# Kernel tuning notes

Measured on AMD Instinct MI355X. Metric: run time of the kernel, lower is better.

Reference implementation:

```python
import jax, jax.numpy as jnp
import numpy as np

N = 50000
E = 1600000
IN_DIM = 256
HID = 64
OUT = 16
NEG_SLOPE = 0.01


def setup_inputs() -> dict:
    key = jax.random.key(0)
    ks = jax.random.split(key, 6)
    local_features = jax.random.normal(ks[0], (N, IN_DIM), dtype=jnp.float32)
    edge_index = jax.random.randint(ks[1], (2, E), 0, N, dtype=jnp.int32)
    W0 = jax.random.normal(ks[2], (IN_DIM, HID), dtype=jnp.float32) * 0.05
    a0 = jax.random.normal(ks[3], (2 * HID, 1), dtype=jnp.float32) * 0.05
    W1 = jax.random.normal(ks[4], (HID, OUT), dtype=jnp.float32) * 0.05
    a1 = jax.random.normal(ks[5], (2 * OUT, 1), dtype=jnp.float32) * 0.05
    return {"local_features": local_features, "edge_index": edge_index,
            "W0": W0, "a0": a0, "W1": W1, "a1": a1}


def _segment_softmax(scores, seg, num_segments):
    # softmax over edges sharing the same row (destination) id
    smax = jax.ops.segment_max(scores, seg, num_segments=num_segments)
    ex = jnp.exp(scores - smax[seg])
    ssum = jax.ops.segment_sum(ex, seg, num_segments=num_segments)
    return ex / ssum[seg]


def _gat_layer(H, row, col, W, a, apply_elu):
    d = W.shape[1]
    Hw = H @ W                                   # [N, d]
    # score_e = leaky_relu([Hw[row] || Hw[col]] @ a) = leaky_relu(pr[row] + pc[col])
    pr = Hw @ a[:d, 0]                           # [N]
    pc = Hw @ a[d:, 0]                           # [N]
    s = pr[row] + pc[col]                        # [E]
    s = jnp.where(s >= 0, s, NEG_SLOPE * s)      # leaky_relu
    att = _segment_softmax(s, row, Hw.shape[0])  # per-row sparse softmax (dim=1)
    # out[row] = sum_e att_e * Hw[col_e]
    out = jax.ops.segment_sum(att[:, None] * Hw[col], row, num_segments=Hw.shape[0])
    if apply_elu:
        out = jnp.where(out > 0, out, jnp.expm1(out))  # elu
    return out


def reference(local_features, edge_index, W0, a0, W1, a1):
    row = edge_index[0]
    col = edge_index[1]
    H = _gat_layer(local_features, row, col, W0, a0, apply_elu=True)
    H = _gat_layer(H, row, col, W1, a1, apply_elu=False)
    return jax.nn.log_softmax(H, axis=1)
```

## Files before the change

kernel.cpp:

```cpp
#include <hip/hip_runtime.h>
#include <hip/hip_bf16.h>
#include <math.h>

#define NN 50000
#define NE 1600000
#define BSH 9
#define BCK 98
#define BCAP 20480

typedef __attribute__((ext_vector_type(8))) short bf16x8;
typedef __attribute__((ext_vector_type(4))) float f32x4;
typedef __attribute__((ext_vector_type(2))) float f32x2;

__device__ __forceinline__ short f2bf(float f) {
    return (short)((__float_as_uint(f) + 0x8000u) >> 16);
}
__device__ __forceinline__ float lo16(unsigned u) { return __uint_as_float(u << 16); }
__device__ __forceinline__ float hi16(unsigned u) { return __uint_as_float(u & 0xffff0000u); }
__device__ __forceinline__ unsigned enc_f(float f) {
    unsigned u = __float_as_uint(f);
    return (u & 0x80000000u) ? ~u : (u | 0x80000000u);
}
__device__ __forceinline__ float dec_f(unsigned e) {
    return (e & 0x80000000u) ? __uint_as_float(e & 0x7FFFFFFFu)
                             : __uint_as_float(~e);
}

__global__ void setup_kernel(int* __restrict__ gcursor, unsigned* __restrict__ maxes,
                             const float* __restrict__ W, ushort* __restrict__ WTg) {
    int b = blockIdx.x;
    int t = threadIdx.x;
    if (b == 0) {
        if (t < BCK) gcursor[t] = t * BCAP;
        if (t < 2) maxes[t] = 0u;
    } else {
        int i = (b - 1) * 256 + t;
        int n = i >> 8, k = i & 255;
        WTg[n * 264 + k] = (ushort)f2bf(W[k * 64 + n]);
    }
}

__global__ void __launch_bounds__(1024) binA_kernel(
        const int* __restrict__ row, const int* __restrict__ col,
        int* __restrict__ gcursor, unsigned* __restrict__ staging) {
    __shared__ unsigned lds_stage[8192];
    __shared__ unsigned lds_addr[8192];
    __shared__ int lds_cnt[128];
    __shared__ int lds_off[128];
    __shared__ int wg_goff[128];
    __shared__ int wtot[2];
    int t = threadIdx.x;
    int lane = t & 63;
    int w = t >> 6;

    for (int cb = blockIdx.x * 8192; cb < NE; cb += gridDim.x * 8192) {
        int cnt_edges = NE - cb; if (cnt_edges > 8192) cnt_edges = 8192;
        if (t < 128) lds_cnt[t] = 0;
        __syncthreads();
        int myb[8]; int mylo[8]; unsigned mypk[8];
        int e0 = cb + t * 8;
        if (t * 8 + 7 < cnt_edges) {
            int4 r0 = *(const int4*)(row + e0);
            int4 r1 = *(const int4*)(row + e0 + 4);
            int4 c0 = *(const int4*)(col + e0);
            int4 c1 = *(const int4*)(col + e0 + 4);
            int rr[8] = {r0.x, r0.y, r0.z, r0.w, r1.x, r1.y, r1.z, r1.w};
            int cc[8] = {c0.x, c0.y, c0.z, c0.w, c1.x, c1.y, c1.z, c1.w};
            #pragma unroll
            for (int i = 0; i < 8; ++i) {
                int b = rr[i] >> BSH;
                myb[i] = b;
                mypk[i] = ((unsigned)(rr[i] & 511) << 16) | (unsigned)cc[i];
                mylo[i] = atomicAdd(&lds_cnt[b], 1);
            }
        } else {
            #pragma unroll
            for (int i = 0; i < 8; ++i) {
                int idx = t * 8 + i;
                myb[i] = -1;
                if (idx < cnt_edges) {
                    int e = cb + idx;
                    int r = row[e], c = col[e];
                    myb[i] = r >> BSH;
                    mypk[i] = ((unsigned)(r & 511) << 16) | (unsigned)c;
                    mylo[i] = atomicAdd(&lds_cnt[myb[i]], 1);
                }
            }
        }
        __syncthreads();
        int v = (t < 128) ? lds_cnt[t] : 0;
        int x = v;
        #pragma unroll
        for (int off = 1; off < 64; off <<= 1) {
            int y = __shfl_up(x, off);
            if (lane >= off) x += y;
        }
        if (t < 128 && lane == 63) wtot[w] = x;
        __syncthreads();
        int add = (w == 1) ? wtot[0] : 0;
        if (t < 128) lds_off[t] = x - v + add;
        if (t < BCK) {
            int cc2 = lds_cnt[t];
            wg_goff[t] = cc2 ? atomicAdd(&gcursor[t], cc2) : 0;
        }
        __syncthreads();
        #pragma unroll
        for (int i = 0; i < 8; ++i) if (myb[i] >= 0) {
            int p = lds_off[myb[i]] + mylo[i];
            lds_stage[p] = mypk[i];
            lds_addr[p] = (unsigned)(wg_goff[myb[i]] + mylo[i]);
        }
        __syncthreads();
        for (int i = t; i < cnt_edges; i += 1024)
            staging[lds_addr[i]] = lds_stage[i];
        __syncthreads();
    }
}

__global__ void __launch_bounds__(1024) binB_kernel(
        const int* __restrict__ gcursor,
        const unsigned* __restrict__ staging,
        int* __restrict__ rowptr,
        ushort* __restrict__ colperm) {
    __shared__ int bsc[128];
    __shared__ int bw[2];
    __shared__ int cur[512];
    __shared__ int wls8[8];
    __shared__ ushort lds_col[BCAP];
    int b = blockIdx.x;
    int t = threadIdx.x;
    int lane = t & 63;
    int w = t >> 6;

    if (t < 128) {
        int v = 0;
        if (t < BCK) {
            v = gcursor[t] - t * BCAP;
            if (v > BCAP) v = BCAP;
        }
        int x = v;
        #pragma unroll
        for (int off = 1; off < 64; off <<= 1) {
            int y = __shfl_up(x, off);
            if (lane >= off) x += y;
        }
        if (lane == 63) bw[w] = x;
        bsc[t] = x - v;
    }
    __syncthreads();
    int gbase = bsc[b] + ((b >= 64) ? bw[0] : 0);
    int cnt = gcursor[b] - b * BCAP;
    if (cnt > BCAP) cnt = BCAP;
    if (b == 0 && t == 0) rowptr[NN] = bw[0] + bw[1];
    int rbase = b << BSH;
    int nrows = NN - rbase; if (nrows > 512) nrows = 512;
    const unsigned* sb = staging + (size_t)b * BCAP;

    unsigned ev[20];
    #pragma unroll
    for (int j = 0; j < 5; ++j) {
        int i0 = t * 4 + j * 4096;
        uint4 val = {0u, 0u, 0u, 0u};
        if (i0 + 3 < cnt) {
            val = *(const uint4*)(sb + i0);
        } else {
            if (i0 + 0 < cnt) val.x = sb[i0 + 0];
            if (i0 + 1 < cnt) val.y = sb[i0 + 1];
            if (i0 + 2 < cnt) val.z = sb[i0 + 2];
            if (i0 + 3 < cnt) val.w = sb[i0 + 3];
        }
        ev[j * 4 + 0] = val.x; ev[j * 4 + 1] = val.y;
        ev[j * 4 + 2] = val.z; ev[j * 4 + 3] = val.w;
    }

    if (t < 512) cur[t] = 0;
    __syncthreads();
    #pragma unroll
    for (int j = 0; j < 5; ++j) {
        #pragma unroll
        for (int l = 0; l < 4; ++l) {
            int idx = t * 4 + j * 4096 + l;
            if (idx < cnt) atomicAdd(&cur[ev[j * 4 + l] >> 16], 1);
        }
    }
    __syncthreads();
    int v = 0, x = 0;
    if (t < 512) {
        v = cur[t];
        x = v;
        #pragma unroll
        for (int off = 1; off < 64; off <<= 1) {
            int y = __shfl_up(x, off);
            if (lane >= off) x += y;
        }
        if (lane == 63) wls8[w] = x;
    }
    __syncthreads();
    if (t < 8) {
        int s = wls8[t];
        #pragma unroll
        for (int off = 1; off < 8; off <<= 1) {
            int y = __shfl_up(s, off, 8);
            if ((t & 7) >= off) s += y;
        }
        wls8[t] = s;
    }
    __syncthreads();
    int excl = 0;
    if (t < 512) {
        excl = x - v + ((w > 0) ? wls8[w - 1] : 0);
        if (t < nrows) rowptr[rbase + t] = gbase + excl;
    }
    __syncthreads();
    if (t < 512) cur[t] = excl;
    __syncthreads();
    #pragma unroll
    for (int j = 0; j < 5; ++j) {
        #pragma unroll
        for (int l = 0; l < 4; ++l) {
            int idx = t * 4 + j * 4096 + l;
            if (idx < cnt) {
                unsigned e = ev[j * 4 + l];
                int pos = atomicAdd(&cur[e >> 16], 1);
                lds_col[pos] = (ushort)(e & 0xFFFFu);
            }
        }
    }
    __syncthreads();
    for (int i = t; i < cnt; i += 1024)
        colperm[gbase + i] = lds_col[i];
}

__global__ void __launch_bounds__(256) gemm0_kernel(
        const float* __restrict__ X,
        const ushort* __restrict__ WTg,
        const float* __restrict__ a,
        __hip_bfloat16* __restrict__ Hwb,
        float* __restrict__ pr,
        float* __restrict__ pc,
        unsigned* __restrict__ max0) {
    __shared__ ushort Wt[64 * 264];
    __shared__ unsigned bmax;
    int tid = threadIdx.x;
    if (tid == 0) bmax = 0u;
    {
        const uint* src = (const uint*)WTg;
        uint* dst = (uint*)Wt;
        for (int i = tid; i < 64 * 132; i += 256) dst[i] = src[i];
    }
    __syncthreads();
    int lane = tid & 63, wid = tid >> 6;
    int c = lane & 15, quad = lane >> 4;
    const ushort* wtp[4];
#pragma unroll
    for (int g = 0; g < 4; ++g) wtp[g] = &Wt[(g * 16 + c) * 264 + quad * 8];
    float aA[4], aB[4];
#pragma unroll
    for (int g = 0; g < 4; ++g) { aA[g] = a[g * 16 + c]; aB[g] = a[64 + g * 16 + c]; }

    int row0 = blockIdx.x * 128 + wid * 16;
    float qmax = -1e30f;

#pragma unroll
    for (int tt = 0; tt < 2; ++tt) {
        int rt = row0 + tt * 64;
        int arow = rt + c; if (arow >= NN) arow = NN - 1;
        const float* xbase = X + (size_t)arow * 256 + quad * 8;
        f32x4 acc[4];
#pragma unroll
        for (int g = 0; g < 4; ++g) acc[g] = (f32x4){0.f, 0.f, 0.f, 0.f};

#pragma unroll
        for (int k0 = 0; k0 < 256; k0 += 32) {
            float4 xa = *(const float4*)(xbase + k0);
            float4 xb = *(const float4*)(xbase + k0 + 4);
            bf16x8 af;
            af[0] = f2bf(xa.x); af[1] = f2bf(xa.y); af[2] = f2bf(xa.z); af[3] = f2bf(xa.w);
            af[4] = f2bf(xb.x); af[5] = f2bf(xb.y); af[6] = f2bf(xb.z); af[7] = f2bf(xb.w);
#pragma unroll
            for (int g = 0; g < 4; ++g) {
                bf16x8 bg = *(const bf16x8*)(wtp[g] + k0);
                acc[g] = __builtin_amdgcn_mfma_f32_16x16x32_bf16(af, bg, acc[g], 0, 0, 0);
            }
        }

#pragma unroll
        for (int r = 0; r < 4; ++r) {
            int row = rt + quad * 4 + r;
            float v0 = acc[0][r], v1 = acc[1][r], v2 = acc[2][r], v3 = acc[3][r];
            if (row < NN) {
                __hip_bfloat16* hp = Hwb + (size_t)row * 64 + c;
                hp[0]  = __float2bfloat16(v0);
                hp[16] = __float2bfloat16(v1);
                hp[32] = __float2bfloat16(v2);
                hp[48] = __float2bfloat16(v3);
            }
            float pv = v0 * aA[0] + v1 * aA[1] + v2 * aA[2] + v3 * aA[3];
            float qv = v0 * aB[0] + v1 * aB[1] + v2 * aB[2] + v3 * aB[3];
#pragma unroll
            for (int off = 8; off; off >>= 1) {
                pv += __shfl_xor(pv, off);
                qv += __shfl_xor(qv, off);
            }
            if (c == 0 && row < NN) { pr[row] = pv; pc[row] = qv; }
            if (row < NN) qmax = fmaxf(qmax, qv);
        }
    }
    qmax = fmaxf(qmax, __shfl_xor(qmax, 16));
    qmax = fmaxf(qmax, __shfl_xor(qmax, 32));
    if (lane == 0) atomicMax(&bmax, enc_f(qmax));
    __syncthreads();
    if (tid == 0) atomicMax(max0, bmax);
}

__global__ void pcmax_kernel(const float* __restrict__ pc, unsigned* __restrict__ out) {
    int i = blockIdx.x * 256 + threadIdx.x;
    float v = (i < NN) ? pc[i] : -1e30f;
    #pragma unroll
    for (int off = 32; off; off >>= 1) v = fmaxf(v, __shfl_xor(v, off));
    if ((threadIdx.x & 63) == 0) atomicMax(out, enc_f(v));
}

__global__ void __launch_bounds__(256) node0_kernel(
        const int* __restrict__ rowptr,
        const ushort* __restrict__ colperm,
        const float* __restrict__ pr,
        const float* __restrict__ pc,
        const unsigned* __restrict__ pcmax,
        const ushort* __restrict__ Hwb,
        const float* __restrict__ W1,
        const float* __restrict__ a1,
        __hip_bfloat16* __restrict__ Hw1b,
        float* __restrict__ pr1,
        float* __restrict__ pc1) {
    __shared__ float W1s[64 * 17];
    __shared__ float a1s[32];
    __shared__ float hbuf[4][64];
    __shared__ unsigned long long wcbuf[4][64];
    int t = threadIdx.x;
    for (int i = t; i < 64 * 16; i += 256)
        W1s[(i >> 4) * 17 + (i & 15)] = W1[i];
    if (t < 32) a1s[t] = a1[t];
    __syncthreads();

    int lane = t & 63;
    int wid = t >> 6;
    int node = blockIdx.x * 4 + wid;
    int k = lane & 7, q = lane >> 3;
    int start = rowptr[node], end = rowptr[node + 1];
    float pri = pr[node];
    float m = pri + dec_f(*pcmax);
    m = (m >= 0.f) ? m : 0.01f * m;

    float wsum = 0.f;
    f32x2 accA = {0.f, 0.f}, accB = {0.f, 0.f};
    f32x2 accC = {0.f, 0.f}, accD = {0.f, 0.f};
    for (int base = start; base < end; base += 64) {
        int n = end - base; if (n > 64) n = 64;
        float wv = 0.f; unsigned cv = 0;
        if (lane < n) {
            cv = (unsigned)colperm[base + lane];
            float s = pri + pc[cv];
            s = (s >= 0.f) ? s : 0.01f * s;
            wv = __expf(s - m);
        }
        wsum += wv;
        wcbuf[wid][lane] = ((unsigned long long)cv << 32) |
                           (unsigned long long)__float_as_uint(wv);
        int iters = (n + 7) >> 3;
        #pragma unroll 4
        for (int jj = 0; jj < iters; ++jj) {
            unsigned long long wc = wcbuf[wid][jj * 8 + q];
            float wj = __uint_as_float((unsigned)wc);
            int cj = (int)(wc >> 32);
            uint4 hv = *(const uint4*)(Hwb + (size_t)cj * 64 + k * 8);
            f32x2 wj2 = {wj, wj};
            accA += wj2 * (f32x2){lo16(hv.x), hi16(hv.x)};
            accB += wj2 * (f32x2){lo16(hv.y), hi16(hv.y)};
            accC += wj2 * (f32x2){lo16(hv.z), hi16(hv.z)};
            accD += wj2 * (f32x2){lo16(hv.w), hi16(hv.w)};
        }
    }
#pragma unroll
    for (int off = 32; off; off >>= 1) wsum += __shfl_xor(wsum, off);
    float ac[8] = {accA.x, accA.y, accB.x, accB.y,
                   accC.x, accC.y, accD.x, accD.y};
#pragma unroll
    for (int j8 = 0; j8 < 8; ++j8) {
        ac[j8] += __shfl_xor(ac[j8], 8);
        ac[j8] += __shfl_xor(ac[j8], 16);
        ac[j8] += __shfl_xor(ac[j8], 32);
    }
    float inv = (wsum > 0.f) ? 1.f / wsum : 0.f;
    float hh[8];
#pragma unroll
    for (int j8 = 0; j8 < 8; ++j8) {
        float h = ac[j8] * inv;
        hh[j8] = (h > 0.f) ? h : (__expf(h) - 1.f);
    }
    if (q == 0) {
        *(float4*)&hbuf[wid][k * 8]     = (float4){hh[0], hh[1], hh[2], hh[3]};
        *(float4*)&hbuf[wid][k * 8 + 4] = (float4){hh[4], hh[5], hh[6], hh[7]};
    }
    int j = lane & 15, p = lane >> 4;
    const float* hbp = hbuf[wid];
    float vj = 0.f;
#pragma unroll
    for (int i = 0; i < 16; ++i) {
        int kk = p * 16 + i;
        vj = fmaf(hbp[kk], W1s[kk * 17 + j], vj);
    }
    vj += __shfl_xor(vj, 16);
    vj += __shfl_xor(vj, 32);
    if (p == 0) Hw1b[(size_t)node * 16 + j] = __float2bfloat16(vj);
    float pv = vj * a1s[j];
    float qv = vj * a1s[16 + j];
#pragma unroll
    for (int off = 8; off; off >>= 1) {
        pv += __shfl_xor(pv, off);
        qv += __shfl_xor(qv, off);
    }
    if (lane == 0) { pr1[node] = pv; pc1[node] = qv; }
}

__global__ void __launch_bounds__(256) node1_kernel(
        const int* __restrict__ rowptr,
        const ushort* __restrict__ colperm,
        const float* __restrict__ pr,
        const float* __restrict__ pc,
        const unsigned* __restrict__ pcmax,
        const ushort* __restrict__ Hwb,
        float* __restrict__ out) {
    __shared__ unsigned long long wcbuf[4][64];
    int lane = threadIdx.x & 63;
    int wid = threadIdx.x >> 6;
    int node = blockIdx.x * 4 + wid;
    int k = lane & 3, q = lane >> 2;
    int start = rowptr[node], end = rowptr[node + 1];
    float pri = pr[node];
    float m = pri + dec_f(*pcmax);
    m = (m >= 0.f) ? m : 0.01f * m;

    float wsum = 0.f;
    f32x2 accA = {0.f, 0.f}, accB = {0.f, 0.f};
    for (int base = start; base < end; base += 64) {
        int n = end - base; if (n > 64) n = 64;
        float wv = 0.f; unsigned cv = 0;
        if (lane < n) {
            cv = (unsigned)colperm[base + lane];
            float s = pri + pc[cv];
            s = (s >= 0.f) ? s : 0.01f * s;
            wv = __expf(s - m);
        }
        wsum += wv;
        wcbuf[wid][lane] = ((unsigned long long)cv << 32) |
                           (unsigned long long)__float_as_uint(wv);
        int iters = (n + 15) >> 4;
        #pragma unroll 4
        for (int jj = 0; jj < iters; ++jj) {
            unsigned long long wc = wcbuf[wid][jj * 16 + q];
            float wj = __uint_as_float((unsigned)wc);
            int cj = (int)(wc >> 32);
            uint2 hv = *(const uint2*)(Hwb + (size_t)cj * 16 + k * 4);
            f32x2 wj2 = {wj, wj};
            accA += wj2 * (f32x2){lo16(hv.x), hi16(hv.x)};
            accB += wj2 * (f32x2){lo16(hv.y), hi16(hv.y)};
        }
    }
#pragma unroll
    for (int off = 32; off; off >>= 1) wsum += __shfl_xor(wsum, off);
    float ac[4] = {accA.x, accA.y, accB.x, accB.y};
#pragma unroll
    for (int j4 = 0; j4 < 4; ++j4) {
        ac[j4] += __shfl_xor(ac[j4], 4);
        ac[j4] += __shfl_xor(ac[j4], 8);
        ac[j4] += __shfl_xor(ac[j4], 16);
        ac[j4] += __shfl_xor(ac[j4], 32);
    }
    float inv = (wsum > 0.f) ? 1.f / wsum : 0.f;
    float v0 = ac[0] * inv, v1 = ac[1] * inv;
    float v2 = ac[2] * inv, v3 = ac[3] * inv;
    float mm = fmaxf(fmaxf(v0, v1), fmaxf(v2, v3));
    mm = fmaxf(mm, __shfl_xor(mm, 1, 4));
    mm = fmaxf(mm, __shfl_xor(mm, 2, 4));
    float ssx = __expf(v0 - mm) + __expf(v1 - mm) + __expf(v2 - mm) + __expf(v3 - mm);
    ssx += __shfl_xor(ssx, 1, 4);
    ssx += __shfl_xor(ssx, 2, 4);
    float lse = mm + __logf(ssx);
    if (q == 0) {
        float4 o = {v0 - lse, v1 - lse, v2 - lse, v3 - lse};
        *(float4*)(out + (size_t)node * 16 + k * 4) = o;
    }
}

extern "C" void kernel_launch(void* const* d_in, const int* in_sizes, int n_in,
                              void* d_out, int out_size, void* d_ws, size_t ws_size,
                              hipStream_t stream) {
    const float* X  = (const float*)d_in[0];
    const int*   ei = (const int*)d_in[1];
    const float* W0 = (const float*)d_in[2];
    const float* a0 = (const float*)d_in[3];
    const float* W1 = (const float*)d_in[4];
    const float* a1 = (const float*)d_in[5];
    float* out = (float*)d_out;

    const int* row = ei;
    const int* col = ei + NE;

    char* wsb = (char*)d_ws;
    size_t off = 0;
    auto alloc = [&](size_t bytes) {
        void* p = wsb + off;
        off += (bytes + 15) & ~(size_t)15;
        return p;
    };
    unsigned* maxes = (unsigned*)alloc(16);
    int* rowptr     = (int*)alloc((NN + 2) * 4);
    int* gcursor    = (int*)alloc(128 * 4);
    unsigned* staging = (unsigned*)alloc((size_t)BCK * BCAP * 4);
    ushort* colperm = (ushort*)alloc((size_t)NE * 2);
    ushort* WTg     = (ushort*)alloc((size_t)64 * 264 * 2);
    __hip_bfloat16* Hw0b = (__hip_bfloat16*)alloc((size_t)NN * 64 * 2);
    float* pr0      = (float*)alloc(NN * 4);
    float* pc0      = (float*)alloc(NN * 4);
    __hip_bfloat16* Hw1b = (__hip_bfloat16*)alloc((size_t)NN * 16 * 2);
    float* pr1      = (float*)alloc(NN * 4);
    float* pc1      = (float*)alloc(NN * 4);

    setup_kernel<<<65, 256, 0, stream>>>(gcursor, maxes, W0, WTg);
    binA_kernel<<<196, 1024, 0, stream>>>(row, col, gcursor, staging);
    binB_kernel<<<BCK, 1024, 0, stream>>>(gcursor, staging, rowptr, colperm);

    gemm0_kernel<<<(NN + 127) / 128, 256, 0, stream>>>(X, WTg, a0, Hw0b, pr0, pc0,
                                                       &maxes[0]);
    node0_kernel<<<NN / 4, 256, 0, stream>>>(rowptr, colperm, pr0, pc0,
                                             &maxes[0], (const ushort*)Hw0b,
                                             W1, a1, Hw1b, pr1, pc1);

    pcmax_kernel<<<(NN + 255) / 256, 256, 0, stream>>>(pc1, &maxes[1]);
    node1_kernel<<<NN / 4, 256, 0, stream>>>(rowptr, colperm, pr1, pc1,
                                             &maxes[1], (const ushort*)Hw1b, out);
}
```

Measured before the change: 213.5 us.

## Fuse GEMM into binning kernel, fold pcmax into node0, narrow node0 gather

The first-layer GEMM blocks now run inside the edge-binning launch, with a union of shared-memory layouts, so GEMM and binning overlap in one grid. The separate pcmax pass is removed: node0 reduces the max of pc1 per block into 32 spread slots, and node1 reduces those slots at start. node0's aggregation moves from 8-lane uint4 loads to 16-lane uint2 loads with fewer accumulators. The aim is fewer launches and better overlap, at the cost of larger GEMM blocks (1024 threads) and extra atomics.

```diff
diff --git a/kernel.cpp b/kernel.cpp
--- a/kernel.cpp
+++ b/kernel.cpp
@@ -7,6 +7,7 @@
 #define BSH 9
 #define BCK 98
 #define BCAP 20480
+#define GEMM_BLKS 98
 
 typedef __attribute__((ext_vector_type(8))) short bf16x8;
 typedef __attribute__((ext_vector_type(4))) float f32x4;
@@ -27,12 +28,14 @@
 }
 
 __global__ void setup_kernel(int* __restrict__ gcursor, unsigned* __restrict__ maxes,
+                             unsigned* __restrict__ max1s,
                              const float* __restrict__ W, ushort* __restrict__ WTg) {
     int b = blockIdx.x;
     int t = threadIdx.x;
     if (b == 0) {
         if (t < BCK) gcursor[t] = t * BCAP;
         if (t < 2) maxes[t] = 0u;
+        for (int i = t; i < 512; i += 256) max1s[i] = 0u;
     } else {
         int i = (b - 1) * 256 + t;
         int n = i >> 8, k = i & 255;
@@ -40,22 +43,114 @@
     }
 }
 
-__global__ void __launch_bounds__(1024) binA_kernel(
+__global__ void __launch_bounds__(1024) gbinA_kernel(
+        const float* __restrict__ X,
+        const ushort* __restrict__ WTg,
+        const float* __restrict__ a,
+        __hip_bfloat16* __restrict__ Hwb,
+        float* __restrict__ pr,
+        float* __restrict__ pc,
+        unsigned* __restrict__ max0,
         const int* __restrict__ row, const int* __restrict__ col,
         int* __restrict__ gcursor, unsigned* __restrict__ staging) {
-    __shared__ unsigned lds_stage[8192];
-    __shared__ unsigned lds_addr[8192];
-    __shared__ int lds_cnt[128];
-    __shared__ int lds_off[128];
-    __shared__ int wg_goff[128];
-    __shared__ int wtot[2];
-    int t = threadIdx.x;
+    __shared__ union SH {
+        struct {
+            unsigned lds_stage[8192];
+            unsigned lds_addr[8192];
+            int lds_cnt[128];
+            int lds_off[128];
+            int wg_goff[128];
+            int wtot[2];
+        } a;
+        struct {
+            ushort Wt[64 * 264];
+            unsigned bmax;
+        } g;
+    } sh;
+    int tid = threadIdx.x;
+
+    if (blockIdx.x < GEMM_BLKS) {
+        if (tid == 0) sh.g.bmax = 0u;
+        {
+            const uint* src = (const uint*)WTg;
+            uint* dst = (uint*)sh.g.Wt;
+            for (int i = tid; i < 64 * 132; i += 1024) dst[i] = src[i];
+        }
+        __syncthreads();
+        int g256 = tid >> 8, t256 = tid & 255;
+        int lane = t256 & 63, wid = t256 >> 6;
+        int c = lane & 15, quad = lane >> 4;
+        const ushort* wtp[4];
+#pragma unroll
+        for (int g = 0; g < 4; ++g) wtp[g] = &sh.g.Wt[(g * 16 + c) * 264 + quad * 8];
+        float aA[4], aB[4];
+#pragma unroll
+        for (int g = 0; g < 4; ++g) { aA[g] = a[g * 16 + c]; aB[g] = a[64 + g * 16 + c]; }
+
+        int row0 = blockIdx.x * 512 + g256 * 128 + wid * 16;
+        float qmax = -1e30f;
+
+#pragma unroll
+        for (int tt = 0; tt < 2; ++tt) {
+            int rt = row0 + tt * 64;
+            int arow = rt + c; if (arow >= NN) arow = NN - 1;
+            const float* xbase = X + (size_t)arow * 256 + quad * 8;
+            f32x4 acc[4];
+#pragma unroll
+            for (int g = 0; g < 4; ++g) acc[g] = (f32x4){0.f, 0.f, 0.f, 0.f};
+
+#pragma unroll
+            for (int k0 = 0; k0 < 256; k0 += 32) {
+                float4 xa = *(const float4*)(xbase + k0);
+                float4 xb = *(const float4*)(xbase + k0 + 4);
+                bf16x8 af;
+                af[0] = f2bf(xa.x); af[1] = f2bf(xa.y); af[2] = f2bf(xa.z); af[3] = f2bf(xa.w);
+                af[4] = f2bf(xb.x); af[5] = f2bf(xb.y); af[6] = f2bf(xb.z); af[7] = f2bf(xb.w);
+#pragma unroll
+                for (int g = 0; g < 4; ++g) {
+                    bf16x8 bg = *(const bf16x8*)(wtp[g] + k0);
+                    acc[g] = __builtin_amdgcn_mfma_f32_16x16x32_bf16(af, bg, acc[g], 0, 0, 0);
+                }
+            }
+
+#pragma unroll
+            for (int r = 0; r < 4; ++r) {
+                int rr = rt + quad * 4 + r;
+                float v0 = acc[0][r], v1 = acc[1][r], v2 = acc[2][r], v3 = acc[3][r];
+                if (rr < NN) {
+                    __hip_bfloat16* hp = Hwb + (size_t)rr * 64 + c;
+                    hp[0]  = __float2bfloat16(v0);
+                    hp[16] = __float2bfloat16(v1);
+                    hp[32] = __float2bfloat16(v2);
+                    hp[48] = __float2bfloat16(v3);
+                }
+                float pv = v0 * aA[0] + v1 * aA[1] + v2 * aA[2] + v3 * aA[3];
+                float qv = v0 * aB[0] + v1 * aB[1] + v2 * aB[2] + v3 * aB[3];
+#pragma unroll
+                for (int off = 8; off; off >>= 1) {
+                    pv += __shfl_xor(pv, off);
+                    qv += __shfl_xor(qv, off);
+                }
+                if (c == 0 && rr < NN) { pr[rr] = pv; pc[rr] = qv; }
+                if (rr < NN) qmax = fmaxf(qmax, qv);
+            }
+        }
+        qmax = fmaxf(qmax, __shfl_xor(qmax, 16));
+        qmax = fmaxf(qmax, __shfl_xor(qmax, 32));
+        if (lane == 0) atomicMax(&sh.g.bmax, enc_f(qmax));
+        __syncthreads();
+        if (tid == 0) atomicMax(max0, sh.g.bmax);
+        return;
+    }
+
+    int t = tid;
     int lane = t & 63;
     int w = t >> 6;
-
-    for (int cb = blockIdx.x * 8192; cb < NE; cb += gridDim.x * 8192) {
+    int nbin = gridDim.x - GEMM_BLKS;
+
+    for (int cb = (blockIdx.x - GEMM_BLKS) * 8192; cb < NE; cb += nbin * 8192) {
         int cnt_edges = NE - cb; if (cnt_edges > 8192) cnt_edges = 8192;
-        if (t < 128) lds_cnt[t] = 0;
+        if (t < 128) sh.a.lds_cnt[t] = 0;
         __syncthreads();
         int myb[8]; int mylo[8]; unsigned mypk[8];
         int e0 = cb + t * 8;
@@ -71,7 +166,7 @@
                 int b = rr[i] >> BSH;
                 myb[i] = b;
                 mypk[i] = ((unsigned)(rr[i] & 511) << 16) | (unsigned)cc[i];
-                mylo[i] = atomicAdd(&lds_cnt[b], 1);
+                mylo[i] = atomicAdd(&sh.a.lds_cnt[b], 1);
             }
         } else {
             #pragma unroll
@@ -83,36 +178,36 @@
                     int r = row[e], c = col[e];
                     myb[i] = r >> BSH;
                     mypk[i] = ((unsigned)(r & 511) << 16) | (unsigned)c;
-                    mylo[i] = atomicAdd(&lds_cnt[myb[i]], 1);
+                    mylo[i] = atomicAdd(&sh.a.lds_cnt[myb[i]], 1);
                 }
             }
         }
         __syncthreads();
-        int v = (t < 128) ? lds_cnt[t] : 0;
+        int v = (t < 128) ? sh.a.lds_cnt[t] : 0;
         int x = v;
         #pragma unroll
         for (int off = 1; off < 64; off <<= 1) {
             int y = __shfl_up(x, off);
             if (lane >= off) x += y;
         }
-        if (t < 128 && lane == 63) wtot[w] = x;
-        __syncthreads();
-        int add = (w == 1) ? wtot[0] : 0;
-        if (t < 128) lds_off[t] = x - v + add;
+        if (t < 128 && lane == 63) sh.a.wtot[w] = x;
+        __syncthreads();
+        int add = (w == 1) ? sh.a.wtot[0] : 0;
+        if (t < 128) sh.a.lds_off[t] = x - v + add;
         if (t < BCK) {
-            int cc2 = lds_cnt[t];
-            wg_goff[t] = cc2 ? atomicAdd(&gcursor[t], cc2) : 0;
+            int cc2 = sh.a.lds_cnt[t];
+            sh.a.wg_goff[t] = cc2 ? atomicAdd(&gcursor[t], cc2) : 0;
         }
         __syncthreads();
         #pragma unroll
         for (int i = 0; i < 8; ++i) if (myb[i] >= 0) {
-            int p = lds_off[myb[i]] + mylo[i];
-            lds_stage[p] = mypk[i];
-            lds_addr[p] = (unsigned)(wg_goff[myb[i]] + mylo[i]);
+            int p = sh.a.lds_off[myb[i]] + mylo[i];
+            sh.a.lds_stage[p] = mypk[i];
+            sh.a.lds_addr[p] = (unsigned)(sh.a.wg_goff[myb[i]] + mylo[i]);
         }
         __syncthreads();
         for (int i = t; i < cnt_edges; i += 1024)
-            staging[lds_addr[i]] = lds_stage[i];
+            staging[sh.a.lds_addr[i]] = sh.a.lds_stage[i];
         __syncthreads();
     }
 }
@@ -231,96 +326,6 @@
         colperm[gbase + i] = lds_col[i];
 }
 
-__global__ void __launch_bounds__(256) gemm0_kernel(
-        const float* __restrict__ X,
-        const ushort* __restrict__ WTg,
-        const float* __restrict__ a,
-        __hip_bfloat16* __restrict__ Hwb,
-        float* __restrict__ pr,
-        float* __restrict__ pc,
-        unsigned* __restrict__ max0) {
-    __shared__ ushort Wt[64 * 264];
-    __shared__ unsigned bmax;
-    int tid = threadIdx.x;
-    if (tid == 0) bmax = 0u;
-    {
-        const uint* src = (const uint*)WTg;
-        uint* dst = (uint*)Wt;
-        for (int i = tid; i < 64 * 132; i += 256) dst[i] = src[i];
-    }
-    __syncthreads();
-    int lane = tid & 63, wid = tid >> 6;
-    int c = lane & 15, quad = lane >> 4;
-    const ushort* wtp[4];
-#pragma unroll
-    for (int g = 0; g < 4; ++g) wtp[g] = &Wt[(g * 16 + c) * 264 + quad * 8];
-    float aA[4], aB[4];
-#pragma unroll
-    for (int g = 0; g < 4; ++g) { aA[g] = a[g * 16 + c]; aB[g] = a[64 + g * 16 + c]; }
-
-    int row0 = blockIdx.x * 128 + wid * 16;
-    float qmax = -1e30f;
-
-#pragma unroll
-    for (int tt = 0; tt < 2; ++tt) {
-        int rt = row0 + tt * 64;
-        int arow = rt + c; if (arow >= NN) arow = NN - 1;
-        const float* xbase = X + (size_t)arow * 256 + quad * 8;
-        f32x4 acc[4];
-#pragma unroll
-        for (int g = 0; g < 4; ++g) acc[g] = (f32x4){0.f, 0.f, 0.f, 0.f};
-
-#pragma unroll
-        for (int k0 = 0; k0 < 256; k0 += 32) {
-            float4 xa = *(const float4*)(xbase + k0);
-            float4 xb = *(const float4*)(xbase + k0 + 4);
-            bf16x8 af;
-            af[0] = f2bf(xa.x); af[1] = f2bf(xa.y); af[2] = f2bf(xa.z); af[3] = f2bf(xa.w);
-            af[4] = f2bf(xb.x); af[5] = f2bf(xb.y); af[6] = f2bf(xb.z); af[7] = f2bf(xb.w);
-#pragma unroll
-            for (int g = 0; g < 4; ++g) {
-                bf16x8 bg = *(const bf16x8*)(wtp[g] + k0);
-                acc[g] = __builtin_amdgcn_mfma_f32_16x16x32_bf16(af, bg, acc[g], 0, 0, 0);
-            }
-        }
-
-#pragma unroll
-        for (int r = 0; r < 4; ++r) {
-            int row = rt + quad * 4 + r;
-            float v0 = acc[0][r], v1 = acc[1][r], v2 = acc[2][r], v3 = acc[3][r];
-            if (row < NN) {
-                __hip_bfloat16* hp = Hwb + (size_t)row * 64 + c;
-                hp[0]  = __float2bfloat16(v0);
-                hp[16] = __float2bfloat16(v1);
-                hp[32] = __float2bfloat16(v2);
-                hp[48] = __float2bfloat16(v3);
-            }
-            float pv = v0 * aA[0] + v1 * aA[1] + v2 * aA[2] + v3 * aA[3];
-            float qv = v0 * aB[0] + v1 * aB[1] + v2 * aB[2] + v3 * aB[3];
-#pragma unroll
-            for (int off = 8; off; off >>= 1) {
-                pv += __shfl_xor(pv, off);
-                qv += __shfl_xor(qv, off);
-            }
-            if (c == 0 && row < NN) { pr[row] = pv; pc[row] = qv; }
-            if (row < NN) qmax = fmaxf(qmax, qv);
-        }
-    }
-    qmax = fmaxf(qmax, __shfl_xor(qmax, 16));
-    qmax = fmaxf(qmax, __shfl_xor(qmax, 32));
-    if (lane == 0) atomicMax(&bmax, enc_f(qmax));
-    __syncthreads();
-    if (tid == 0) atomicMax(max0, bmax);
-}
-
-__global__ void pcmax_kernel(const float* __restrict__ pc, unsigned* __restrict__ out) {
-    int i = blockIdx.x * 256 + threadIdx.x;
-    float v = (i < NN) ? pc[i] : -1e30f;
-    #pragma unroll
-    for (int off = 32; off; off >>= 1) v = fmaxf(v, __shfl_xor(v, off));
-    if ((threadIdx.x & 63) == 0) atomicMax(out, enc_f(v));
-}
-
 __global__ void __launch_bounds__(256) node0_kernel(
         const int* __restrict__ rowptr,
         const ushort* __restrict__ colperm,
@@ -332,12 +337,15 @@
         const float* __restrict__ a1,
         __hip_bfloat16* __restrict__ Hw1b,
         float* __restrict__ pr1,
-        float* __restrict__ pc1) {
+        float* __restrict__ pc1,
+        unsigned* __restrict__ max1s) {
     __shared__ float W1s[64 * 17];
     __shared__ float a1s[32];
     __shared__ float hbuf[4][64];
     __shared__ unsigned long long wcbuf[4][64];
+    __shared__ unsigned bmax1;
     int t = threadIdx.x;
+    if (t == 0) bmax1 = 0u;
     for (int i = t; i < 64 * 16; i += 256)
         W1s[(i >> 4) * 17 + (i & 15)] = W1[i];
     if (t < 32) a1s[t] = a1[t];
@@ -346,7 +354,7 @@
     int lane = t & 63;
     int wid = t >> 6;
     int node = blockIdx.x * 4 + wid;
-    int k = lane & 7, q = lane >> 3;
+    int k = lane & 15, q = lane >> 4;
     int start = rowptr[node], end = rowptr[node + 1];
     float pri = pr[node];
     float m = pri + dec_f(*pcmax);
@@ -354,7 +362,6 @@
 
     float wsum = 0.f;
     f32x2 accA = {0.f, 0.f}, accB = {0.f, 0.f};
-    f32x2 accC = {0.f, 0.f}, accD = {0.f, 0.f};
     for (int base = start; base < end; base += 64) {
         int n = end - base; if (n > 64) n = 64;
         float wv = 0.f; unsigned cv = 0;
@@ -367,40 +374,36 @@
         wsum += wv;
         wcbuf[wid][lane] = ((unsigned long long)cv << 32) |
                            (unsigned long long)__float_as_uint(wv);
-        int iters = (n + 7) >> 3;
+        int iters = (n + 3) >> 2;
         #pragma unroll 4
         for (int jj = 0; jj < iters; ++jj) {
-            unsigned long long wc = wcbuf[wid][jj * 8 + q];
+            unsigned long long wc = wcbuf[wid][jj * 4 + q];
             float wj = __uint_as_float((unsigned)wc);
             int cj = (int)(wc >> 32);
-            uint4 hv = *(const uint4*)(Hwb + (size_t)cj * 64 + k * 8);
+            uint2 hv = *(const uint2*)(Hwb + (size_t)cj * 64 + k * 4);
             f32x2 wj2 = {wj, wj};
-            accA += wj2 * (f32x2){lo16(hv.x), hi16(hv.x)};
-            accB += wj2 * (f32x2){lo16(hv.y), hi16(hv.y)};
-            accC += wj2 * (f32x2){lo16(hv.z), hi16(hv.z)};
-            accD += wj2 * (f32x2){lo16(hv.w), hi16(hv.w)};
+            f32x2 h01 = {lo16(hv.x), hi16(hv.x)};
+            f32x2 h23 = {lo16(hv.y), hi16(hv.y)};
+            accA += wj2 * h01;
+            accB += wj2 * h23;
         }
     }
 #pragma unroll
     for (int off = 32; off; off >>= 1) wsum += __shfl_xor(wsum, off);
-    float ac[8] = {accA.x, accA.y, accB.x, accB.y,
-                   accC.x, accC.y, accD.x, accD.y};
-#pragma unroll
-    for (int j8 = 0; j8 < 8; ++j8) {
-        ac[j8] += __shfl_xor(ac[j8], 8);
-        ac[j8] += __shfl_xor(ac[j8], 16);
-        ac[j8] += __shfl_xor(ac[j8], 32);
-    }
+    float acc0 = accA.x, acc1 = accA.y, acc2 = accB.x, acc3 = accB.y;
+    acc0 += __shfl_xor(acc0, 16); acc0 += __shfl_xor(acc0, 32);
+    acc1 += __shfl_xor(acc1, 16); acc1 += __shfl_xor(acc1, 32);
+    acc2 += __shfl_xor(acc2, 16); acc2 += __shfl_xor(acc2, 32);
+    acc3 += __shfl_xor(acc3, 16); acc3 += __shfl_xor(acc3, 32);
+
     float inv = (wsum > 0.f) ? 1.f / wsum : 0.f;
-    float hh[8];
-#pragma unroll
-    for (int j8 = 0; j8 < 8; ++j8) {
-        float h = ac[j8] * inv;
-        hh[j8] = (h > 0.f) ? h : (__expf(h) - 1.f);
-    }
+    float h0 = acc0 * inv; h0 = (h0 > 0.f) ? h0 : (__expf(h0) - 1.f);
+    float h1 = acc1 * inv; h1 = (h1 > 0.f) ? h1 : (__expf(h1) - 1.f);
+    float h2 = acc2 * inv; h2 = (h2 > 0.f) ? h2 : (__expf(h2) - 1.f);
+    float h3 = acc3 * inv; h3 = (h3 > 0.f) ? h3 : (__expf(h3) - 1.f);
     if (q == 0) {
-        *(float4*)&hbuf[wid][k * 8]     = (float4){hh[0], hh[1], hh[2], hh[3]};
-        *(float4*)&hbuf[wid][k * 8 + 4] = (float4){hh[4], hh[5], hh[6], hh[7]};
+        float4 hh = {h0, h1, h2, h3};
+        *(float4*)&hbuf[wid][k * 4] = hh;
     }
     int j = lane & 15, p = lane >> 4;
     const float* hbp = hbuf[wid];
@@ -420,7 +423,12 @@
         pv += __shfl_xor(pv, off);
         qv += __shfl_xor(qv, off);
     }
-    if (lane == 0) { pr1[node] = pv; pc1[node] = qv; }
+    if (lane == 0) {
+        pr1[node] = pv; pc1[node] = qv;
+        atomicMax(&bmax1, enc_f(qv));
+    }
+    __syncthreads();
+    if (t == 0) atomicMax(&max1s[(blockIdx.x & 31) * 16], bmax1);
 }
 
 __global__ void __launch_bounds__(256) node1_kernel(
@@ -428,17 +436,29 @@
         const ushort* __restrict__ colperm,
         const float* __restrict__ pr,
         const float* __restrict__ pc,
-        const unsigned* __restrict__ pcmax,
+        const unsigned* __restrict__ max1s,
         const ushort* __restrict__ Hwb,
         float* __restrict__ out) {
     __shared__ unsigned long long wcbuf[4][64];
-    int lane = threadIdx.x & 63;
-    int wid = threadIdx.x >> 6;
+    __shared__ unsigned gmx;
+    int t = threadIdx.x;
+    if (t < 32) {
+        unsigned v = max1s[t * 16];
+        #pragma unroll
+        for (int off = 16; off; off >>= 1) {
+            unsigned o = (unsigned)__shfl_xor((int)v, off, 32);
+            v = (v > o) ? v : o;
+        }
+        if (t == 0) gmx = v;
+    }
+    __syncthreads();
+    int lane = t & 63;
+    int wid = t >> 6;
     int node = blockIdx.x * 4 + wid;
     int k = lane & 3, q = lane >> 2;
     int start = rowptr[node], end = rowptr[node + 1];
     float pri = pr[node];
-    float m = pri + dec_f(*pcmax);
+    float m = pri + dec_f(gmx);
     m = (m >= 0.f) ? m : 0.01f * m;
 
     float wsum = 0.f;
@@ -515,6 +535,7 @@
         return p;
     };
     unsigned* maxes = (unsigned*)alloc(16);
+    unsigned* max1s = (unsigned*)alloc(512 * 4);
     int* rowptr     = (int*)alloc((NN + 2) * 4);
     int* gcursor    = (int*)alloc(128 * 4);
     unsigned* staging = (unsigned*)alloc((size_t)BCK * BCAP * 4);
@@ -527,17 +548,16 @@
     float* pr1      = (float*)alloc(NN * 4);
     float* pc1      = (float*)alloc(NN * 4);
 
-    setup_kernel<<<65, 256, 0, stream>>>(gcursor, maxes, W0, WTg);
-    binA_kernel<<<196, 1024, 0, stream>>>(row, col, gcursor, staging);
+    setup_kernel<<<65, 256, 0, stream>>>(gcursor, maxes, max1s, W0, WTg);
+    gbinA_kernel<<<GEMM_BLKS + 196, 1024, 0, stream>>>(X, WTg, a0, Hw0b, pr0, pc0,
+                                                       &maxes[0], row, col,
+                                                       gcursor, staging);
     binB_kernel<<<BCK, 1024, 0, stream>>>(gcursor, staging, rowptr, colperm);
 
-    gemm0_kernel<<<(NN + 127) / 128, 256, 0, stream>>>(X, WTg, a0, Hw0b, pr0, pc0,
-                                                       &maxes[0]);
     node0_kernel<<<NN / 4, 256, 0, stream>>>(rowptr, colperm, pr0, pc0,
                                              &maxes[0], (const ushort*)Hw0b,
-                                             W1, a1, Hw1b, pr1, pc1);
-
-    pcmax_kernel<<<(NN + 255) / 256, 256, 0, stream>>>(pc1, &maxes[1]);
+                                             W1, a1, Hw1b, pr1, pc1, max1s);
+
     node1_kernel<<<NN / 4, 256, 0, stream>>>(rowptr, colperm, pr1, pc1,
-                                             &maxes[1], (const ushort*)Hw1b, out);
-}
+                                             max1s, (const ushort*)Hw1b, out);
+}
```

After: 211.4 us. Within noise of the previous version (-1.0%).
